# Kernel optimization log

Measured on AMD Instinct MI355X. Metric: run time of the kernel, lower is better.

The kernel has to match this reference:

```python
import jax, jax.numpy as jnp
import numpy as np

TOP_K = 2  # top_routing

def setup_inputs() -> dict:
    key = jax.random.key(0)
    ks = jax.random.split(key, 8)
    B, D, O, E = 2048, 1024, 1024, 8
    H = D * 10  # hidden_dim hard-coded as input_dim*10
    s_d = 1.0 / np.sqrt(D)
    s_h = 1.0 / np.sqrt(H)
    return {
        "x1": jax.random.normal(ks[0], (B, D), jnp.float32),
        "x2": jax.random.normal(ks[1], (B, D), jnp.float32),
        "gate_w": jax.random.uniform(ks[2], (E, D), jnp.float32, -s_d, s_d),
        "gate_b": jax.random.uniform(ks[3], (E,), jnp.float32, -s_d, s_d),
        "fc1_w": jax.random.uniform(ks[4], (E, H, D), jnp.float32, -s_d, s_d),
        "fc1_b": jax.random.uniform(ks[5], (E, H), jnp.float32, -s_d, s_d),
        "fc2_w": jax.random.uniform(ks[6], (E, O, H), jnp.float32, -s_h, s_h),
        "fc2_b": jax.random.uniform(ks[7], (E, O), jnp.float32, -s_h, s_h),
    }


def reference(x1, x2, gate_w, gate_b, fc1_w, fc1_b, fc2_w, fc2_b):
    # Gate: softmax over experts, then top-k sparsify (values kept, rest zeroed)
    gate_logits = x1 @ gate_w.T + gate_b                    # [B, E]
    gate_probs = jax.nn.softmax(gate_logits, axis=1)
    top_vals, top_idx = jax.lax.top_k(gate_probs, TOP_K)    # [B, K]
    B = gate_probs.shape[0]
    rows = jnp.arange(B)[:, None]
    gate_probs = jnp.zeros_like(gate_probs).at[rows, top_idx].set(top_vals)

    # All experts run densely on x2 (faithful to the original Python loop)
    hidden = jnp.einsum('bd,ehd->beh', x2, fc1_w) + fc1_b   # [B, E, H]
    hidden = jax.nn.relu(hidden)
    expert_out = jnp.einsum('beh,eoh->beo', hidden, fc2_w) + fc2_b  # [B, E, O]

    # bmm(gate_probs[:,None,:], expert_out).squeeze(1)
    return jnp.einsum('be,beo->bo', gate_probs, expert_out)  # [B, O]
```

## Files before the change

### kernel.cpp

```cpp
#include <hip/hip_runtime.h>
#include <hip/hip_fp16.h>
#include <stdint.h>

#define BTOK 2048
#define DIM 1024
#define ODIM 1024
#define NEXP 8
#define HID 10240
#define CAP 2048
#define KSPL 8

typedef _Float16 half8 __attribute__((ext_vector_type(8)));
typedef __fp16 fp16x2 __attribute__((ext_vector_type(2)));
typedef float floatx4 __attribute__((ext_vector_type(4)));

#define WS_HIDDEN_OFF 0
#define WS_COUNTS_OFF 83886080UL
#define WS_TOKENS_OFF 83886144UL
#define WS_PROBS_OFF  83951680UL
#define WS_NEEDED     84017216UL

#define BAR()                                         \
    do {                                              \
        asm volatile("s_waitcnt lgkmcnt(0)");         \
        __builtin_amdgcn_sched_barrier(0);            \
        __builtin_amdgcn_s_barrier();                 \
        __builtin_amdgcn_sched_barrier(0);            \
    } while (0)

__global__ void gate_kernel(const float* __restrict__ x1,
                            const float* __restrict__ gate_w,
                            const float* __restrict__ gate_b,
                            int* counts, int* tokens, float* probs) {
    int b = blockIdx.x;
    int lane = threadIdx.x;
    const float* xr = x1 + (size_t)b * DIM;
    float acc[NEXP];
#pragma unroll
    for (int e = 0; e < NEXP; e++) acc[e] = 0.f;
    for (int i = 0; i < DIM / 64; i++) {
        int d = lane + i * 64;
        float xv = xr[d];
#pragma unroll
        for (int e = 0; e < NEXP; e++) acc[e] += xv * gate_w[e * DIM + d];
    }
#pragma unroll
    for (int e = 0; e < NEXP; e++)
        for (int off = 32; off > 0; off >>= 1) acc[e] += __shfl_xor(acc[e], off);
    if (lane == 0) {
        float l[NEXP], m = -1e30f;
#pragma unroll
        for (int e = 0; e < NEXP; e++) { l[e] = acc[e] + gate_b[e]; m = fmaxf(m, l[e]); }
        float p[NEXP], s = 0.f;
#pragma unroll
        for (int e = 0; e < NEXP; e++) { p[e] = expf(l[e] - m); s += p[e]; }
        float inv = 1.f / s;
        int e0 = 0; float v0 = p[0];
#pragma unroll
        for (int e = 1; e < NEXP; e++) if (p[e] > v0) { v0 = p[e]; e0 = e; }
        int e1 = -1; float v1 = -1.f;
#pragma unroll
        for (int e = 0; e < NEXP; e++) if (e != e0 && p[e] > v1) { v1 = p[e]; e1 = e; }
        int pos0 = atomicAdd(&counts[e0], 1);
        tokens[e0 * CAP + pos0] = b; probs[e0 * CAP + pos0] = v0 * inv;
        int pos1 = atomicAdd(&counts[e1], 1);
        tokens[e1 * CAP + pos1] = b; probs[e1 * CAP + pos1] = v1 * inv;
    }
}

#define BM 256
#define BN 256
#define BK 32

__device__ __forceinline__ half8 cvt8(float4 a, float4 b) {
    union { fp16x2 h2[4]; half8 h8; } u;
    u.h2[0] = __builtin_amdgcn_cvt_pkrtz(a.x, a.y);
    u.h2[1] = __builtin_amdgcn_cvt_pkrtz(a.z, a.w);
    u.h2[2] = __builtin_amdgcn_cvt_pkrtz(b.x, b.y);
    u.h2[3] = __builtin_amdgcn_cvt_pkrtz(b.z, b.w);
    return u.h8;
}

__device__ __forceinline__ int expert_off(const int* __restrict__ counts, int e) {
    int off = 0;
#pragma unroll
    for (int i = 0; i < NEXP; i++) {
        int c = counts[i];
        off += (i < e) ? c : 0;
    }
    return off;
}

__global__ __launch_bounds__(1024, 4) void gemm1_kernel(
    const float* __restrict__ x2, const float* __restrict__ fc1_w,
    const float* __restrict__ fc1_b, const int* __restrict__ counts,
    const int* __restrict__ tokens, _Float16* __restrict__ hidden) {
    int d = blockIdx.x;
    int e = d & 7;
    int rest = d >> 3;
    int nt = rest >> 3;
    int mt = rest & 7;

    int cnt = counts[e];
    int m0 = mt * BM;
    if (m0 >= cnt) return;
    int n0 = nt * BN;
    int off = expert_off(counts, e);

    __shared__ __align__(16) _Float16 As[2 * BM * BK];
    __shared__ __align__(16) _Float16 Bs[2 * BN * BK];

    int t = threadIdx.x;
    int lane = t & 63, wave = t >> 6;
    int waveM = wave >> 2, waveN = wave & 3;
    int fr = lane & 15, q = lane >> 4;

    int srow = t >> 2;
    int sg = t & 3;
    int swz = sg ^ ((srow >> 1) & 3);
    int arow = min(m0 + srow, cnt - 1);
    const float* ag = x2 + (size_t)tokens[e * CAP + arow] * DIM + sg * 8;
    const float* bg = fc1_w + ((size_t)e * HID + n0 + srow) * DIM + sg * 8;
    _Float16* aw = As + srow * BK + swz * 8;
    _Float16* bw = Bs + srow * BK + swz * 8;

    floatx4 acc[4][4];
#pragma unroll
    for (int mi = 0; mi < 4; mi++)
#pragma unroll
        for (int ni = 0; ni < 4; ni++) acc[mi][ni] = (floatx4){0.f, 0.f, 0.f, 0.f};

    float4 pa0, pa1, pb0, pb1;
    auto LOADT = [&](int kt) {
        const float* a_ = ag + kt * BK;
        const float* b_ = bg + kt * BK;
        pa0 = *(const float4*)a_;
        pa1 = *(const float4*)(a_ + 4);
        pb0 = *(const float4*)b_;
        pb1 = *(const float4*)(b_ + 4);
    };
    auto WRITET = [&](int buf) {
        *(volatile half8*)(aw + buf * (BM * BK)) = cvt8(pa0, pa1);
        *(volatile half8*)(bw + buf * (BN * BK)) = cvt8(pb0, pb1);
    };

    const int KT = DIM / BK;
    LOADT(0);
    WRITET(0);
    LOADT(1);
    BAR();
    int cur = 0;
    for (int kt = 0; kt < KT; kt++) {
        half8 af[4], bf[4];
        const _Float16* Ar = As + cur * (BM * BK);
        const _Float16* Br = Bs + cur * (BN * BK);
#pragma unroll
        for (int mi = 0; mi < 4; mi++) {
            int row = waveM * 64 + mi * 16 + fr;
            af[mi] = *(const half8*)(Ar + row * BK + ((q ^ ((row >> 1) & 3)) * 8));
        }
#pragma unroll
        for (int ni = 0; ni < 4; ni++) {
            int row = waveN * 64 + ni * 16 + fr;
            bf[ni] = *(const half8*)(Br + row * BK + ((q ^ ((row >> 1) & 3)) * 8));
        }
#pragma unroll
        for (int mi = 0; mi < 4; mi++)
#pragma unroll
            for (int ni = 0; ni < 4; ni++)
                acc[mi][ni] = __builtin_amdgcn_mfma_f32_16x16x32_f16(
                    af[mi], bf[ni], acc[mi][ni], 0, 0, 0);
        if (kt + 1 < KT) WRITET(cur ^ 1);
        if (kt + 2 < KT) LOADT(kt + 2);
        BAR();
        cur ^= 1;
    }
#pragma unroll
    for (int ni = 0; ni < 4; ni++) {
        int col = n0 + waveN * 64 + ni * 16 + fr;
        float bias = fc1_b[e * HID + col];
#pragma unroll
        for (int mi = 0; mi < 4; mi++) {
#pragma unroll
            for (int r = 0; r < 4; r++) {
                int rl = m0 + waveM * 64 + mi * 16 + q * 4 + r;
                if (rl < cnt) {
                    float v = fmaxf(acc[mi][ni][r] + bias, 0.f);
                    hidden[(size_t)(off + rl) * HID + col] = (_Float16)v;
                }
            }
        }
    }
}

__global__ __launch_bounds__(1024, 4) void gemm2_kernel(
    const _Float16* __restrict__ hidden, const float* __restrict__ fc2_w,
    const float* __restrict__ fc2_b, const int* __restrict__ counts,
    const int* __restrict__ tokens, const float* __restrict__ probs,
    float* __restrict__ out) {
    int d = blockIdx.x;
    int e = d & 7;
    int rest = d >> 3;
    int mt = rest & 7;
    int nt = (rest >> 3) & 3;
    int ks = rest >> 5;

    int cnt = counts[e];
    int m0 = mt * BM;
    if (m0 >= cnt) return;
    int n0 = nt * BN;
    int off = expert_off(counts, e);
    int k0 = ks * (HID / KSPL);

    __shared__ __align__(16) _Float16 As[2 * BM * BK];
    __shared__ __align__(16) _Float16 Bs[2 * BN * BK];

    int t = threadIdx.x;
    int lane = t & 63, wave = t >> 6;
    int waveM = wave >> 2, waveN = wave & 3;
    int fr = lane & 15, q = lane >> 4;

    int srow = t >> 2;
    int sg = t & 3;
    int swz = sg ^ ((srow >> 1) & 3);
    int arow = min(m0 + srow, cnt - 1);
    const _Float16* ag = hidden + (size_t)(off + arow) * HID + k0 + sg * 8;
    const float* bg = fc2_w + ((size_t)e * ODIM + n0 + srow) * HID + k0 + sg * 8;
    _Float16* aw = As + srow * BK + swz * 8;
    _Float16* bw = Bs + srow * BK + swz * 8;

    floatx4 acc[4][4];
#pragma unroll
    for (int mi = 0; mi < 4; mi++)
#pragma unroll
        for (int ni = 0; ni < 4; ni++) acc[mi][ni] = (floatx4){0.f, 0.f, 0.f, 0.f};

    half8 pa;
    float4 pb0, pb1;
    auto LOADT = [&](int kt) {
        pa = *(const half8*)(ag + kt * BK);
        const float* b_ = bg + kt * BK;
        pb0 = *(const float4*)b_;
        pb1 = *(const float4*)(b_ + 4);
    };
    auto WRITET = [&](int buf) {
        *(volatile half8*)(aw + buf * (BM * BK)) = pa;
        *(volatile half8*)(bw + buf * (BN * BK)) = cvt8(pb0, pb1);
    };

    const int KT = (HID / KSPL) / BK;
    LOADT(0);
    WRITET(0);
    LOADT(1);
    BAR();
    int cur = 0;
    for (int kt = 0; kt < KT; kt++) {
        half8 af[4], bf[4];
        const _Float16* Ar = As + cur * (BM * BK);
        const _Float16* Br = Bs + cur * (BN * BK);
#pragma unroll
        for (int mi = 0; mi < 4; mi++) {
            int row = waveM * 64 + mi * 16 + fr;
            af[mi] = *(const half8*)(Ar + row * BK + ((q ^ ((row >> 1) & 3)) * 8));
        }
#pragma unroll
        for (int ni = 0; ni < 4; ni++) {
            int row = waveN * 64 + ni * 16 + fr;
            bf[ni] = *(const half8*)(Br + row * BK + ((q ^ ((row >> 1) & 3)) * 8));
        }
#pragma unroll
        for (int mi = 0; mi < 4; mi++)
#pragma unroll
            for (int ni = 0; ni < 4; ni++)
                acc[mi][ni] = __builtin_amdgcn_mfma_f32_16x16x32_f16(
                    af[mi], bf[ni], acc[mi][ni], 0, 0, 0);
        if (kt + 1 < KT) WRITET(cur ^ 1);
        if (kt + 2 < KT) LOADT(kt + 2);
        BAR();
        cur ^= 1;
    }
#pragma unroll
    for (int ni = 0; ni < 4; ni++) {
        int col = n0 + waveN * 64 + ni * 16 + fr;
        float bias = (ks == 0) ? fc2_b[e * ODIM + col] : 0.f;
#pragma unroll
        for (int mi = 0; mi < 4; mi++) {
#pragma unroll
            for (int r = 0; r < 4; r++) {
                int rl = m0 + waveM * 64 + mi * 16 + q * 4 + r;
                if (rl < cnt) {
                    float p = probs[e * CAP + rl];
                    int tok = tokens[e * CAP + rl];
                    atomicAdd(&out[(size_t)tok * ODIM + col],
                              p * (acc[mi][ni][r] + bias));
                }
            }
        }
    }
}

extern "C" void kernel_launch(void* const* d_in, const int* in_sizes, int n_in,
                              void* d_out, int out_size, void* d_ws, size_t ws_size,
                              hipStream_t stream) {
    if (ws_size < WS_NEEDED) return;
    const float* x1 = (const float*)d_in[0];
    const float* x2 = (const float*)d_in[1];
    const float* gate_w = (const float*)d_in[2];
    const float* gate_b = (const float*)d_in[3];
    const float* fc1_w = (const float*)d_in[4];
    const float* fc1_b = (const float*)d_in[5];
    const float* fc2_w = (const float*)d_in[6];
    const float* fc2_b = (const float*)d_in[7];
    float* out = (float*)d_out;
    char* ws = (char*)d_ws;
    _Float16* hidden = (_Float16*)(ws + WS_HIDDEN_OFF);
    int* counts = (int*)(ws + WS_COUNTS_OFF);
    int* tokens = (int*)(ws + WS_TOKENS_OFF);
    float* probs = (float*)(ws + WS_PROBS_OFF);

    (void)hipMemsetAsync(counts, 0, 2 * NEXP * sizeof(int), stream);
    (void)hipMemsetAsync(d_out, 0, (size_t)out_size * sizeof(float), stream);
    gate_kernel<<<BTOK, 64, 0, stream>>>(x1, gate_w, gate_b, counts, tokens, probs);
    gemm1_kernel<<<(CAP / BM) * (HID / BN) * NEXP, 1024, 0, stream>>>(
        x2, fc1_w, fc1_b, counts, tokens, hidden);
    gemm2_kernel<<<(CAP / BM) * (ODIM / BN) * NEXP * KSPL, 1024, 0, stream>>>(
        hidden, fc2_w, fc2_b, counts, tokens, probs, out);
}
```

Before: 1.241 ms.

## Pre-convert weights to fp16 and stream tiles via direct global-to-LDS loads

```diff
diff --git a/kernel.cpp b/kernel.cpp
--- a/kernel.cpp
+++ b/kernel.cpp
@@ -8,25 +8,54 @@
 #define NEXP 8
 #define HID 10240
 #define CAP 2048
-#define KSPL 8
 
 typedef _Float16 half8 __attribute__((ext_vector_type(8)));
 typedef __fp16 fp16x2 __attribute__((ext_vector_type(2)));
 typedef float floatx4 __attribute__((ext_vector_type(4)));
 
-#define WS_HIDDEN_OFF 0
+#define WS_HIDDEN_OFF 0UL
 #define WS_COUNTS_OFF 83886080UL
 #define WS_TOKENS_OFF 83886144UL
 #define WS_PROBS_OFF  83951680UL
-#define WS_NEEDED     84017216UL
-
-#define BAR()                                         \
-    do {                                              \
-        asm volatile("s_waitcnt lgkmcnt(0)");         \
-        __builtin_amdgcn_sched_barrier(0);            \
-        __builtin_amdgcn_s_barrier();                 \
-        __builtin_amdgcn_sched_barrier(0);            \
-    } while (0)
+#define WS_SMALL      84017216UL
+#define WS_FC1H_OFF   84017216UL
+#define WS_FC2H_OFF   251789376UL
+#define WS_X2H_OFF    419561536UL
+#define WS_BIG        423755840UL
+
+typedef __attribute__((address_space(1))) const unsigned int guint;
+typedef __attribute__((address_space(3))) unsigned int luint;
+__device__ __forceinline__ void gload16(const void* g, void* l) {
+    __builtin_amdgcn_global_load_lds((guint*)g, (luint*)l, 16, 0, 0);
+}
+
+__device__ __forceinline__ half8 cvt8(float4 a, float4 b) {
+    union { fp16x2 h2[4]; half8 h8; } u;
+    u.h2[0] = __builtin_amdgcn_cvt_pkrtz(a.x, a.y);
+    u.h2[1] = __builtin_amdgcn_cvt_pkrtz(a.z, a.w);
+    u.h2[2] = __builtin_amdgcn_cvt_pkrtz(b.x, b.y);
+    u.h2[3] = __builtin_amdgcn_cvt_pkrtz(b.z, b.w);
+    return u.h8;
+}
+
+__device__ __forceinline__ int expert_off(const int* __restrict__ counts, int e) {
+    int off = 0;
+#pragma unroll
+    for (int i = 0; i < NEXP; i++) {
+        int c = counts[i];
+        off += (i < e) ? c : 0;
+    }
+    return off;
+}
+
+__global__ void cvt_f32_f16(const float* __restrict__ s, _Float16* __restrict__ d,
+                            long n8) {
+    long i = (long)blockIdx.x * blockDim.x + threadIdx.x;
+    long stride = (long)gridDim.x * blockDim.x;
+    const float4* s4 = (const float4*)s;
+    half8* d8 = (half8*)d;
+    for (; i < n8; i += stride) d8[i] = cvt8(s4[2 * i], s4[2 * i + 1]);
+}
 
 __global__ void gate_kernel(const float* __restrict__ x1,
                             const float* __restrict__ gate_w,
@@ -68,30 +97,210 @@
     }
 }
 
-#define BM 256
-#define BN 256
-#define BK 32
-
-__device__ __forceinline__ half8 cvt8(float4 a, float4 b) {
-    union { fp16x2 h2[4]; half8 h8; } u;
-    u.h2[0] = __builtin_amdgcn_cvt_pkrtz(a.x, a.y);
-    u.h2[1] = __builtin_amdgcn_cvt_pkrtz(a.z, a.w);
-    u.h2[2] = __builtin_amdgcn_cvt_pkrtz(b.x, b.y);
-    u.h2[3] = __builtin_amdgcn_cvt_pkrtz(b.z, b.w);
-    return u.h8;
-}
-
-__device__ __forceinline__ int expert_off(const int* __restrict__ counts, int e) {
-    int off = 0;
-#pragma unroll
-    for (int i = 0; i < NEXP; i++) {
-        int c = counts[i];
-        off += (i < e) ? c : 0;
-    }
-    return off;
-}
-
-__global__ __launch_bounds__(1024, 4) void gemm1_kernel(
+
+__global__ __launch_bounds__(512, 6) void gemm1_h(
+    const _Float16* __restrict__ x2h, const _Float16* __restrict__ w1h,
+    const float* __restrict__ fc1_b, const int* __restrict__ counts,
+    const int* __restrict__ tokens, _Float16* __restrict__ hidden) {
+    int d = blockIdx.x;
+    int e = d & 7;
+    int rest = d >> 3;
+    int mt = rest & 7;
+    int nt = rest >> 3;
+
+    int cnt = counts[e];
+    int m0 = mt * 256;
+    if (m0 >= cnt) return;
+    int n0 = nt * 128;
+    int off = expert_off(counts, e);
+
+    __shared__ __align__(16) _Float16 As[2 * 256 * 32];
+    __shared__ __align__(16) _Float16 Bs[2 * 128 * 32];
+
+    int t = threadIdx.x, lane = t & 63, wave = t >> 6;
+    int waveM = wave >> 1, waveN = wave & 1;
+    int fr = lane & 15, q = lane >> 4;
+    int l4 = lane >> 2, sl = lane & 3;
+
+    const _Float16* agp[2];
+#pragma unroll
+    for (int c = 0; c < 2; c++) {
+        int row = (2 * wave + c) * 16 + l4;
+        int g = sl ^ ((row >> 1) & 3);
+        int ar = min(m0 + row, cnt - 1);
+        agp[c] = x2h + (size_t)tokens[e * CAP + ar] * DIM + g * 8;
+    }
+    int brow = wave * 16 + l4;
+    int bg = sl ^ ((brow >> 1) & 3);
+    const _Float16* bgp = w1h + ((size_t)e * HID + n0 + brow) * DIM + bg * 8;
+
+    floatx4 acc[4][4];
+#pragma unroll
+    for (int mi = 0; mi < 4; mi++)
+#pragma unroll
+        for (int ni = 0; ni < 4; ni++) acc[mi][ni] = (floatx4){0.f, 0.f, 0.f, 0.f};
+
+    auto ISSUE = [&](int buf, int kt) {
+        int ko = kt * 32;
+#pragma unroll
+        for (int c = 0; c < 2; c++)
+            gload16(agp[c] + ko, (char*)As + buf * 16384 + (2 * wave + c) * 1024);
+        gload16(bgp + ko, (char*)Bs + buf * 8192 + wave * 1024);
+    };
+
+    const int KT = DIM / 32;
+    ISSUE(0, 0);
+    __syncthreads();
+    int cur = 0;
+    for (int kt = 0; kt < KT; kt++) {
+        if (kt + 1 < KT) ISSUE(cur ^ 1, kt + 1);
+        half8 af[4], bf[4];
+        const _Float16* Ar = As + cur * 8192;
+        const _Float16* Br = Bs + cur * 4096;
+#pragma unroll
+        for (int mi = 0; mi < 4; mi++) {
+            int row = waveM * 64 + mi * 16 + fr;
+            af[mi] = *(const half8*)(Ar + row * 32 + ((q ^ ((row >> 1) & 3)) * 8));
+        }
+#pragma unroll
+        for (int ni = 0; ni < 4; ni++) {
+            int row = waveN * 64 + ni * 16 + fr;
+            bf[ni] = *(const half8*)(Br + row * 32 + ((q ^ ((row >> 1) & 3)) * 8));
+        }
+#pragma unroll
+        for (int mi = 0; mi < 4; mi++)
+#pragma unroll
+            for (int ni = 0; ni < 4; ni++)
+                acc[mi][ni] = __builtin_amdgcn_mfma_f32_16x16x32_f16(
+                    af[mi], bf[ni], acc[mi][ni], 0, 0, 0);
+        __syncthreads();
+        cur ^= 1;
+    }
+#pragma unroll
+    for (int ni = 0; ni < 4; ni++) {
+        int col = n0 + waveN * 64 + ni * 16 + fr;
+        float bias = fc1_b[e * HID + col];
+#pragma unroll
+        for (int mi = 0; mi < 4; mi++) {
+#pragma unroll
+            for (int r = 0; r < 4; r++) {
+                int rl = m0 + waveM * 64 + mi * 16 + q * 4 + r;
+                if (rl < cnt) {
+                    float v = fmaxf(acc[mi][ni][r] + bias, 0.f);
+                    hidden[(size_t)(off + rl) * HID + col] = (_Float16)v;
+                }
+            }
+        }
+    }
+}
+
+__global__ __launch_bounds__(512, 6) void gemm2_h(
+    const _Float16* __restrict__ hidden, const _Float16* __restrict__ w2h,
+    const float* __restrict__ fc2_b, const int* __restrict__ counts,
+    const int* __restrict__ tokens, const float* __restrict__ probs,
+    float* __restrict__ out) {
+    int d = blockIdx.x;
+    int e = d & 7;
+    int rest = d >> 3;
+    int mt = rest & 7;
+    int nt = (rest >> 3) & 7;
+    int ks = rest >> 6;
+
+    int cnt = counts[e];
+    int m0 = mt * 256;
+    if (m0 >= cnt) return;
+    int n0 = nt * 128;
+    int off = expert_off(counts, e);
+    int k0 = ks * (HID / 8);
+
+    __shared__ __align__(16) _Float16 As[2 * 256 * 32];
+    __shared__ __align__(16) _Float16 Bs[2 * 128 * 32];
+
+    int t = threadIdx.x, lane = t & 63, wave = t >> 6;
+    int waveM = wave >> 1, waveN = wave & 1;
+    int fr = lane & 15, q = lane >> 4;
+    int l4 = lane >> 2, sl = lane & 3;
+
+    const _Float16* agp[2];
+#pragma unroll
+    for (int c = 0; c < 2; c++) {
+        int row = (2 * wave + c) * 16 + l4;
+        int g = sl ^ ((row >> 1) & 3);
+        int ar = min(m0 + row, cnt - 1);
+        agp[c] = hidden + (size_t)(off + ar) * HID + k0 + g * 8;
+    }
+    int brow = wave * 16 + l4;
+    int bg = sl ^ ((brow >> 1) & 3);
+    const _Float16* bgp = w2h + ((size_t)e * ODIM + n0 + brow) * HID + k0 + bg * 8;
+
+    floatx4 acc[4][4];
+#pragma unroll
+    for (int mi = 0; mi < 4; mi++)
+#pragma unroll
+        for (int ni = 0; ni < 4; ni++) acc[mi][ni] = (floatx4){0.f, 0.f, 0.f, 0.f};
+
+    auto ISSUE = [&](int buf, int kt) {
+        int ko = kt * 32;
+#pragma unroll
+        for (int c = 0; c < 2; c++)
+            gload16(agp[c] + ko, (char*)As + buf * 16384 + (2 * wave + c) * 1024);
+        gload16(bgp + ko, (char*)Bs + buf * 8192 + wave * 1024);
+    };
+
+    const int KT = (HID / 8) / 32;
+    ISSUE(0, 0);
+    __syncthreads();
+    int cur = 0;
+    for (int kt = 0; kt < KT; kt++) {
+        if (kt + 1 < KT) ISSUE(cur ^ 1, kt + 1);
+        half8 af[4], bf[4];
+        const _Float16* Ar = As + cur * 8192;
+        const _Float16* Br = Bs + cur * 4096;
+#pragma unroll
+        for (int mi = 0; mi < 4; mi++) {
+            int row = waveM * 64 + mi * 16 + fr;
+            af[mi] = *(const half8*)(Ar + row * 32 + ((q ^ ((row >> 1) & 3)) * 8));
+        }
+#pragma unroll
+        for (int ni = 0; ni < 4; ni++) {
+            int row = waveN * 64 + ni * 16 + fr;
+            bf[ni] = *(const half8*)(Br + row * 32 + ((q ^ ((row >> 1) & 3)) * 8));
+        }
+#pragma unroll
+        for (int mi = 0; mi < 4; mi++)
+#pragma unroll
+            for (int ni = 0; ni < 4; ni++)
+                acc[mi][ni] = __builtin_amdgcn_mfma_f32_16x16x32_f16(
+                    af[mi], bf[ni], acc[mi][ni], 0, 0, 0);
+        __syncthreads();
+        cur ^= 1;
+    }
+#pragma unroll
+    for (int ni = 0; ni < 4; ni++) {
+        int col = n0 + waveN * 64 + ni * 16 + fr;
+        float bias = (ks == 0) ? fc2_b[e * ODIM + col] : 0.f;
+#pragma unroll
+        for (int mi = 0; mi < 4; mi++) {
+#pragma unroll
+            for (int r = 0; r < 4; r++) {
+                int rl = m0 + waveM * 64 + mi * 16 + q * 4 + r;
+                if (rl < cnt) {
+                    float p = probs[e * CAP + rl];
+                    int tok = tokens[e * CAP + rl];
+                    atomicAdd(&out[(size_t)tok * ODIM + col],
+                              p * (acc[mi][ni][r] + bias));
+                }
+            }
+        }
+    }
+}
+
+#define BMf 256
+#define BNf 256
+#define BKf 32
+#define KSPLf 8
+
+__global__ __launch_bounds__(1024, 4) void gemm1_f(
     const float* __restrict__ x2, const float* __restrict__ fc1_w,
     const float* __restrict__ fc1_b, const int* __restrict__ counts,
     const int* __restrict__ tokens, _Float16* __restrict__ hidden) {
@@ -102,13 +311,13 @@
     int mt = rest & 7;
 
     int cnt = counts[e];
-    int m0 = mt * BM;
+    int m0 = mt * BMf;
     if (m0 >= cnt) return;
-    int n0 = nt * BN;
+    int n0 = nt * BNf;
     int off = expert_off(counts, e);
 
-    __shared__ __align__(16) _Float16 As[2 * BM * BK];
-    __shared__ __align__(16) _Float16 Bs[2 * BN * BK];
+    __shared__ __align__(16) _Float16 As[2 * BMf * BKf];
+    __shared__ __align__(16) _Float16 Bs[2 * BNf * BKf];
 
     int t = threadIdx.x;
     int lane = t & 63, wave = t >> 6;
@@ -121,8 +330,8 @@
     int arow = min(m0 + srow, cnt - 1);
     const float* ag = x2 + (size_t)tokens[e * CAP + arow] * DIM + sg * 8;
     const float* bg = fc1_w + ((size_t)e * HID + n0 + srow) * DIM + sg * 8;
-    _Float16* aw = As + srow * BK + swz * 8;
-    _Float16* bw = Bs + srow * BK + swz * 8;
+    _Float16* aw = As + srow * BKf + swz * 8;
+    _Float16* bw = Bs + srow * BKf + swz * 8;
 
     floatx4 acc[4][4];
 #pragma unroll
@@ -132,47 +341,48 @@
 
     float4 pa0, pa1, pb0, pb1;
     auto LOADT = [&](int kt) {
-        const float* a_ = ag + kt * BK;
-        const float* b_ = bg + kt * BK;
+        const float* a_ = ag + kt * BKf;
+        const float* b_ = bg + kt * BKf;
         pa0 = *(const float4*)a_;
         pa1 = *(const float4*)(a_ + 4);
         pb0 = *(const float4*)b_;
         pb1 = *(const float4*)(b_ + 4);
     };
     auto WRITET = [&](int buf) {
-        *(volatile half8*)(aw + buf * (BM * BK)) = cvt8(pa0, pa1);
-        *(volatile half8*)(bw + buf * (BN * BK)) = cvt8(pb0, pb1);
+        *(half8*)(aw + buf * (BMf * BKf)) = cvt8(pa0, pa1);
+        *(half8*)(bw + buf * (BNf * BKf)) = cvt8(pb0, pb1);
     };
 
-    const int KT = DIM / BK;
+    const int KT = DIM / BKf;
     LOADT(0);
     WRITET(0);
     LOADT(1);
-    BAR();
+    __syncthreads();
     int cur = 0;
     for (int kt = 0; kt < KT; kt++) {
         half8 af[4], bf[4];
-        const _Float16* Ar = As + cur * (BM * BK);
-        const _Float16* Br = Bs + cur * (BN * BK);
+        const _Float16* Ar = As + cur * (BMf * BKf);
+        const _Float16* Br = Bs + cur * (BNf * BKf);
 #pragma unroll
         for (int mi = 0; mi < 4; mi++) {
             int row = waveM * 64 + mi * 16 + fr;
-            af[mi] = *(const half8*)(Ar + row * BK + ((q ^ ((row >> 1) & 3)) * 8));
+            af[mi] = *(const half8*)(Ar + row * BKf + ((q ^ ((row >> 1) & 3)) * 8));
         }
 #pragma unroll
         for (int ni = 0; ni < 4; ni++) {
             int row = waveN * 64 + ni * 16 + fr;
-            bf[ni] = *(const half8*)(Br + row * BK + ((q ^ ((row >> 1) & 3)) * 8));
-        }
+            bf[ni] = *(const half8*)(Br + row * BKf + ((q ^ ((row >> 1) & 3)) * 8));
+        }
+        __syncthreads();
+        if (kt + 1 < KT) WRITET(cur ^ 1);
+        if (kt + 2 < KT) LOADT(kt + 2);
 #pragma unroll
         for (int mi = 0; mi < 4; mi++)
 #pragma unroll
             for (int ni = 0; ni < 4; ni++)
                 acc[mi][ni] = __builtin_amdgcn_mfma_f32_16x16x32_f16(
                     af[mi], bf[ni], acc[mi][ni], 0, 0, 0);
-        if (kt + 1 < KT) WRITET(cur ^ 1);
-        if (kt + 2 < KT) LOADT(kt + 2);
-        BAR();
+        __syncthreads();
         cur ^= 1;
     }
 #pragma unroll
@@ -193,7 +403,7 @@
     }
 }
 
-__global__ __launch_bounds__(1024, 4) void gemm2_kernel(
+__global__ __launch_bounds__(1024, 4) void gemm2_f(
     const _Float16* __restrict__ hidden, const float* __restrict__ fc2_w,
     const float* __restrict__ fc2_b, const int* __restrict__ counts,
     const int* __restrict__ tokens, const float* __restrict__ probs,
@@ -206,14 +416,14 @@
     int ks = rest >> 5;
 
     int cnt = counts[e];
-    int m0 = mt * BM;
+    int m0 = mt * BMf;
     if (m0 >= cnt) return;
-    int n0 = nt * BN;
+    int n0 = nt * BNf;
     int off = expert_off(counts, e);
-    int k0 = ks * (HID / KSPL);
-
-    __shared__ __align__(16) _Float16 As[2 * BM * BK];
-    __shared__ __align__(16) _Float16 Bs[2 * BN * BK];
+    int k0 = ks * (HID / KSPLf);
+
+    __shared__ __align__(16) _Float16 As[2 * BMf * BKf];
+    __shared__ __align__(16) _Float16 Bs[2 * BNf * BKf];
 
     int t = threadIdx.x;
     int lane = t & 63, wave = t >> 6;
@@ -226,8 +436,8 @@
     int arow = min(m0 + srow, cnt - 1);
     const _Float16* ag = hidden + (size_t)(off + arow) * HID + k0 + sg * 8;
     const float* bg = fc2_w + ((size_t)e * ODIM + n0 + srow) * HID + k0 + sg * 8;
-    _Float16* aw = As + srow * BK + swz * 8;
-    _Float16* bw = Bs + srow * BK + swz * 8;
+    _Float16* aw = As + srow * BKf + swz * 8;
+    _Float16* bw = Bs + srow * BKf + swz * 8;
 
     floatx4 acc[4][4];
 #pragma unroll
@@ -238,45 +448,46 @@
     half8 pa;
     float4 pb0, pb1;
     auto LOADT = [&](int kt) {
-        pa = *(const half8*)(ag + kt * BK);
-        const float* b_ = bg + kt * BK;
+        pa = *(const half8*)(ag + kt * BKf);
+        const float* b_ = bg + kt * BKf;
         pb0 = *(const float4*)b_;
         pb1 = *(const float4*)(b_ + 4);
     };
     auto WRITET = [&](int buf) {
-        *(volatile half8*)(aw + buf * (BM * BK)) = pa;
-        *(volatile half8*)(bw + buf * (BN * BK)) = cvt8(pb0, pb1);
+        *(half8*)(aw + buf * (BMf * BKf)) = pa;
+        *(half8*)(bw + buf * (BNf * BKf)) = cvt8(pb0, pb1);
     };
 
-    const int KT = (HID / KSPL) / BK;
+    const int KT = (HID / KSPLf) / BKf;
     LOADT(0);
     WRITET(0);
     LOADT(1);
-    BAR();
+    __syncthreads();
     int cur = 0;
     for (int kt = 0; kt < KT; kt++) {
         half8 af[4], bf[4];
-        const _Float16* Ar = As + cur * (BM * BK);
-        const _Float16* Br = Bs + cur * (BN * BK);
+        const _Float16* Ar = As + cur * (BMf * BKf);
+        const _Float16* Br = Bs + cur * (BNf * BKf);
 #pragma unroll
         for (int mi = 0; mi < 4; mi++) {
             int row = waveM * 64 + mi * 16 + fr;
-            af[mi] = *(const half8*)(Ar + row * BK + ((q ^ ((row >> 1) & 3)) * 8));
+            af[mi] = *(const half8*)(Ar + row * BKf + ((q ^ ((row >> 1) & 3)) * 8));
         }
 #pragma unroll
         for (int ni = 0; ni < 4; ni++) {
             int row = waveN * 64 + ni * 16 + fr;
-            bf[ni] = *(const half8*)(Br + row * BK + ((q ^ ((row >> 1) & 3)) * 8));
-        }
+            bf[ni] = *(const half8*)(Br + row * BKf + ((q ^ ((row >> 1) & 3)) * 8));
+        }
+        __syncthreads();
+        if (kt + 1 < KT) WRITET(cur ^ 1);
+        if (kt + 2 < KT) LOADT(kt + 2);
 #pragma unroll
         for (int mi = 0; mi < 4; mi++)
 #pragma unroll
             for (int ni = 0; ni < 4; ni++)
                 acc[mi][ni] = __builtin_amdgcn_mfma_f32_16x16x32_f16(
                     af[mi], bf[ni], acc[mi][ni], 0, 0, 0);
-        if (kt + 1 < KT) WRITET(cur ^ 1);
-        if (kt + 2 < KT) LOADT(kt + 2);
-        BAR();
+        __syncthreads();
         cur ^= 1;
     }
 #pragma unroll
@@ -302,7 +513,7 @@
 extern "C" void kernel_launch(void* const* d_in, const int* in_sizes, int n_in,
                               void* d_out, int out_size, void* d_ws, size_t ws_size,
                               hipStream_t stream) {
-    if (ws_size < WS_NEEDED) return;
+    if (ws_size < WS_SMALL) return;
     const float* x1 = (const float*)d_in[0];
     const float* x2 = (const float*)d_in[1];
     const float* gate_w = (const float*)d_in[2];
@@ -321,8 +532,22 @@
     (void)hipMemsetAsync(counts, 0, 2 * NEXP * sizeof(int), stream);
     (void)hipMemsetAsync(d_out, 0, (size_t)out_size * sizeof(float), stream);
     gate_kernel<<<BTOK, 64, 0, stream>>>(x1, gate_w, gate_b, counts, tokens, probs);
-    gemm1_kernel<<<(CAP / BM) * (HID / BN) * NEXP, 1024, 0, stream>>>(
-        x2, fc1_w, fc1_b, counts, tokens, hidden);
-    gemm2_kernel<<<(CAP / BM) * (ODIM / BN) * NEXP * KSPL, 1024, 0, stream>>>(
-        hidden, fc2_w, fc2_b, counts, tokens, probs, out);
-}
+
+    if (ws_size >= WS_BIG) {
+        _Float16* fc1h = (_Float16*)(ws + WS_FC1H_OFF);
+        _Float16* fc2h = (_Float16*)(ws + WS_FC2H_OFF);
+        _Float16* x2h = (_Float16*)(ws + WS_X2H_OFF);
+        cvt_f32_f16<<<2048, 256, 0, stream>>>(fc1_w, fc1h, 10485760L);
+        cvt_f32_f16<<<2048, 256, 0, stream>>>(fc2_w, fc2h, 10485760L);
+        cvt_f32_f16<<<512, 256, 0, stream>>>(x2, x2h, 262144L);
+        gemm1_h<<<8 * 80 * 8, 512, 0, stream>>>(x2h, fc1h, fc1_b, counts, tokens,
+                                                hidden);
+        gemm2_h<<<8 * 8 * 8 * 8, 512, 0, stream>>>(hidden, fc2h, fc2_b, counts,
+                                                   tokens, probs, out);
+    } else {
+        gemm1_f<<<(CAP / BMf) * (HID / BNf) * NEXP, 1024, 0, stream>>>(
+            x2, fc1_w, fc1_b, counts, tokens, hidden);
+        gemm2_f<<<(CAP / BMf) * (ODIM / BNf) * NEXP * KSPLf, 1024, 0, stream>>>(
+            hidden, fc2_w, fc2_b, counts, tokens, probs, out);
+    }
+}
```

Result: slower. 2.556 ms (+106.0%).
